# Kernel optimization log

Measured on AMD Instinct MI355X. Metric: run time of the kernel, lower is better.

Reference implementation:

```python
import jax, jax.numpy as jnp
import numpy as np

B, S, D = 8, 2048, 128
ALPHA = 1.0


def setup_inputs() -> dict:
    key = jax.random.key(0)
    kq, kk, kv, kl = jax.random.split(key, 4)
    q = jax.random.normal(kq, (B, S, D), dtype=jnp.float32)
    k = jax.random.normal(kk, (B, S, D), dtype=jnp.float32)
    v = jax.random.normal(kv, (B, S, D), dtype=jnp.float32)
    # ragged valid-length mask [B, S, 1] (1.0 for valid tokens) to exercise masked softmax
    lengths = jax.random.randint(kl, (B,), S // 2, S + 1)
    rep_mask = (jnp.arange(S)[None, :] < lengths[:, None]).astype(jnp.float32)[:, :, None]
    return {"q": q, "k": k, "v": v, "rep_mask": rep_mask}


def _masked_softmax(vec, mask):
    # faithful to torch masked_softmax with dim=2 (last axis)
    masked_vec = vec * mask
    max_vec = jnp.max(masked_vec, axis=2, keepdims=True)
    exps = jnp.exp(masked_vec - max_vec)
    masked_exps = exps * mask
    masked_sums = jnp.sum(masked_exps, axis=2, keepdims=True)
    masked_sums = masked_sums + (masked_sums == 0).astype(vec.dtype)
    return masked_exps / (masked_sums + 1e-20)


def reference(q, k, v, rep_mask):
    seq_len = q.shape[1]
    scale = jnp.sqrt(jnp.asarray(q.shape[2], dtype=q.dtype))
    attn = jnp.einsum('bsd,btd->bst', q, k) / scale  # [B,S,S]
    # rep mask tile: outer product of per-token validity
    mask = rep_mask * jnp.swapaxes(rep_mask, 1, 2)  # [B,S,S]
    # forward directional mask: strictly lower triangular (diagonal=-1)
    direct = jnp.tril(jnp.ones((seq_len, seq_len), dtype=q.dtype), k=-1)[None]
    mask = mask * direct
    # distance bias: -|i-j|
    idx = jnp.arange(seq_len)
    dist = -jnp.abs(idx[:, None] - idx[None, :]).astype(q.dtype)[None]
    attn = attn + ALPHA * dist
    attn = _masked_softmax(attn, mask)
    out = jnp.einsum('bst,btd->bsd', attn, v)  # [B,S,D]
    return (out, attn)
```

## Files before the change

### kernel.cpp

```cpp
#include <hip/hip_runtime.h>

#define NBATCH 8
#define S 2048
#define D 128
#define BQ 32
#define BK 64
#define NKT 32
#define NQT 64
#define INV_SQRT_D 0.08838834764831845f

typedef __bf16 bfv8 __attribute__((ext_vector_type(8)));
typedef float f32x4 __attribute__((ext_vector_type(4)));

__device__ __forceinline__ f32x4 mfma16(bfv8 a, bfv8 b, f32x4 c) {
    return __builtin_amdgcn_mfma_f32_16x16x32_bf16(a, b, c, 0, 0, 0);
}

__device__ __forceinline__ unsigned int pack2(float lo, float hi) {
    unsigned short a = __builtin_bit_cast(unsigned short, (__bf16)lo);
    unsigned short b = __builtin_bit_cast(unsigned short, (__bf16)hi);
    return (unsigned int)a | ((unsigned int)b << 16);
}

__device__ __forceinline__ void gload_lds16(const void* g, void* l) {
    __builtin_amdgcn_global_load_lds(
        (const __attribute__((address_space(1))) unsigned int*)g,
        (__attribute__((address_space(3))) unsigned int*)l, 16, 0, 0);
}

__global__ __launch_bounds__(256) void prep_kernel(
    const float* __restrict__ k, const float* __restrict__ v,
    __bf16* __restrict__ kb, __bf16* __restrict__ vtb)
{
    __shared__ __bf16 lds[64][132];
    const int bidx = blockIdx.x;
    const int tid  = threadIdx.x;

    if (bidx < 1024) {
        const int t   = bidx * 256 + tid;
        const int b   = t >> 15;
        const int kt  = (t >> 10) & 31;
        const int row = (t >> 4) & 63;
        const int u   = t & 15;
        const float4 f0 = *(const float4*)&k[((size_t)(b * S + kt * 64 + row)) * D + u * 8];
        const float4 f1 = *(const float4*)&k[((size_t)(b * S + kt * 64 + row)) * D + u * 8 + 4];
        bfv8 o;
        o[0] = (__bf16)f0.x; o[1] = (__bf16)f0.y; o[2] = (__bf16)f0.z; o[3] = (__bf16)f0.w;
        o[4] = (__bf16)f1.x; o[5] = (__bf16)f1.y; o[6] = (__bf16)f1.z; o[7] = (__bf16)f1.w;
        const size_t unit = ((size_t)((b * 32 + kt) * 64 + row)) * 16 + (u ^ (row & 7));
        *(bfv8*)&kb[unit * 8] = o;
    } else {
        const int vb = bidx - 1024;
        const int b  = vb >> 5;
        const int kt = vb & 31;
#pragma unroll
        for (int p = 0; p < 8; ++p) {
            const int idx = p * 256 + tid;
            const int kv  = idx >> 5;
            const int c4  = idx & 31;
            const float4 f = *(const float4*)&v[((size_t)(b * S + kt * 64 + kv)) * D + c4 * 4];
            __bf16* dst = &lds[kv][c4 * 4];
            dst[0] = (__bf16)f.x; dst[1] = (__bf16)f.y; dst[2] = (__bf16)f.z; dst[3] = (__bf16)f.w;
        }
        __syncthreads();
#pragma unroll
        for (int p = 0; p < 4; ++p) {
            const int idx = p * 256 + tid;
            const int d   = idx >> 3;
            const int u   = idx & 7;
            bfv8 o;
#pragma unroll
            for (int j = 0; j < 8; ++j) o[j] = lds[u * 8 + j][d];
            const size_t unit = ((size_t)((b * 32 + kt) * 128 + d)) * 8 + (u ^ (d & 7));
            *(bfv8*)&vtb[unit * 8] = o;
        }
    }
}

__global__ __launch_bounds__(256) void attn_main(
    const float* __restrict__ q, const float* __restrict__ rep,
    const __bf16* __restrict__ kb, const __bf16* __restrict__ vtb,
    float* __restrict__ out, float* __restrict__ attn)
{
    __shared__ __attribute__((aligned(16))) __bf16 slots[4][8192];
    __shared__ __attribute__((aligned(16))) __bf16 qs[BQ][136];
    __shared__ __attribute__((aligned(16))) __bf16 ps[BQ][72];
    __shared__ float redsum[2][2][16];
    __shared__ float dinv_lds[BQ];

    const int tid  = threadIdx.x;
    const int bid  = blockIdx.x;
    const int b    = bid & 7;
    const int g    = bid >> 3;
    const int qt   = (g < 32) ? (63 - g) : (g - 32);
    const int i0   = qt * BQ;
    const int NT   = ((qt * BQ + (BQ - 2)) >> 6) + 1;

    const int lane = tid & 63;
    const int w    = tid >> 6;
    const int rg   = w >> 1;
    const int ch   = w & 1;
    const int lr   = lane & 15;
    const int lg   = lane >> 4;

    auto stageK = [&](int kt, int slot) {
        const char* src = (const char*)kb + (((size_t)(b * 32 + kt)) << 14);
        char* dst = (char*)&slots[slot][0];
#pragma unroll
        for (int i2 = 0; i2 < 4; ++i2) {
            const int n0 = (w * 4 + i2) * 64;
            gload_lds16(src + (size_t)(n0 + lane) * 16, dst + (size_t)n0 * 16);
        }
    };
    auto stageV = [&](int kt, int slot) {
        const char* src = (const char*)vtb + (((size_t)(b * 32 + kt)) << 14);
        char* dst = (char*)&slots[slot][0];
#pragma unroll
        for (int i2 = 0; i2 < 4; ++i2) {
            const int n0 = (w * 4 + i2) * 64;
            gload_lds16(src + (size_t)(n0 + lane) * 16, dst + (size_t)n0 * 16);
        }
    };
    auto kfrag = [&](int slot, int row, int u) -> bfv8 {
        return *(const bfv8*)&slots[slot][(row * 16 + (u ^ (row & 7))) * 8];
    };
    auto vfrag = [&](int slot, int drow, int u) -> bfv8 {
        return *(const bfv8*)&slots[slot][(drow * 8 + (u ^ (drow & 7))) * 8];
    };

    stageK(0, 0);
    stageV(0, 2);

    for (int c = tid; c < BQ * 16; c += 256) {
        const int row = c >> 4, c8 = c & 15;
        const float4 f0 = *(const float4*)&q[((size_t)(b * S + i0 + row)) * D + c8 * 8];
        const float4 f1 = *(const float4*)&q[((size_t)(b * S + i0 + row)) * D + c8 * 8 + 4];
        bfv8 t;
        t[0] = (__bf16)f0.x; t[1] = (__bf16)f0.y; t[2] = (__bf16)f0.z; t[3] = (__bf16)f0.w;
        t[4] = (__bf16)f1.x; t[5] = (__bf16)f1.y; t[6] = (__bf16)f1.z; t[7] = (__bf16)f1.w;
        *(bfv8*)&qs[row][c8 * 8] = t;
    }

    unsigned int vm0 = 0, vm1 = 0;
    for (int kt = 0; kt < NT; ++kt) {
        const unsigned int t0 = (rep[(size_t)b * S + kt * BK + ch * 32 + lr]      > 0.5f) ? 1u : 0u;
        const unsigned int t1 = (rep[(size_t)b * S + kt * BK + ch * 32 + 16 + lr] > 0.5f) ? 1u : 0u;
        vm0 |= t0 << kt;
        vm1 |= t1 << kt;
    }

    int  i_r[4];
    bool bi[4];
#pragma unroll
    for (int r = 0; r < 4; ++r) {
        i_r[r] = i0 + rg * 16 + lg * 4 + r;
        bi[r]  = rep[(size_t)b * S + i_r[r]] > 0.5f;
    }
    __syncthreads();

    bfv8 qa[4];
#pragma unroll
    for (int ks = 0; ks < 4; ++ks)
        qa[ks] = *(const bfv8*)&qs[rg * 16 + lr][ks * 32 + lg * 8];

    const int krow = ch * 32 + lr;
    const int csw  = krow & 7;
    int koff[4];
#pragma unroll
    for (int ks = 0; ks < 4; ++ks)
        koff[ks] = krow * 256 + (((ks * 4 + lg) ^ csw) << 4);
    const char* kbb = (const char*)kb + (((size_t)(b * 32)) << 14);

    float lsum[4] = {0.f, 0.f, 0.f, 0.f};
#pragma unroll 2
    for (int kt = 0; kt < NT; ++kt) {
        const char* tp = kbb + ((size_t)kt << 14);
        bfv8 kf0[4], kf1[4];
#pragma unroll
        for (int ks = 0; ks < 4; ++ks) {
            kf0[ks] = *(const bfv8*)(tp + koff[ks]);
            kf1[ks] = *(const bfv8*)(tp + koff[ks] + 4096);
        }
        f32x4 acc0 = {0.f, 0.f, 0.f, 0.f}, acc1 = {0.f, 0.f, 0.f, 0.f};
#pragma unroll
        for (int ks = 0; ks < 4; ++ks) {
            acc0 = mfma16(qa[ks], kf0[ks], acc0);
            acc1 = mfma16(qa[ks], kf1[ks], acc1);
        }

        const int j0 = kt * BK + ch * 32 + lr;
        const int j1 = j0 + 16;
        const bool vj0 = (vm0 >> kt) & 1;
        const bool vj1 = (vm1 >> kt) & 1;
#pragma unroll
        for (int r = 0; r < 4; ++r) {
            const int i = i_r[r];
            const float p0 = (bi[r] && vj0 && (j0 < i))
                ? __expf(acc0[r] * INV_SQRT_D - (float)(i - j0)) : 0.f;
            const float p1 = (bi[r] && vj1 && (j1 < i))
                ? __expf(acc1[r] * INV_SQRT_D - (float)(i - j1)) : 0.f;
            lsum[r] += p0 + p1;
        }
    }

#pragma unroll
    for (int r = 0; r < 4; ++r) {
        lsum[r] += __shfl_xor(lsum[r], 1);
        lsum[r] += __shfl_xor(lsum[r], 2);
        lsum[r] += __shfl_xor(lsum[r], 4);
        lsum[r] += __shfl_xor(lsum[r], 8);
    }
    if (lr == 0) {
#pragma unroll
        for (int r = 0; r < 4; ++r) redsum[rg][ch][lg * 4 + r] = lsum[r];
    }
    __syncthreads();
    if (tid < BQ) {
        const float s = redsum[tid >> 4][0][tid & 15] + redsum[tid >> 4][1][tid & 15];
        dinv_lds[tid] = 1.f / (s + ((s == 0.f) ? 1.f : 0.f) + 1e-20f);
    }
    __syncthreads();

    float dinv[4];
#pragma unroll
    for (int r = 0; r < 4; ++r) dinv[r] = dinv_lds[rg * 16 + lg * 4 + r];

    f32x4 oacc[4];
#pragma unroll
    for (int nf = 0; nf < 4; ++nf) oacc[nf] = (f32x4){0.f, 0.f, 0.f, 0.f};

    for (int kt = 0; kt < NT; ++kt) {
        const int kslot = kt & 1;
        const int vslot = 2 + (kt & 1);

        if (kt + 1 < NT) { stageK(kt + 1, (kt + 1) & 1); stageV(kt + 1, 2 + ((kt + 1) & 1)); }

        f32x4 acc0 = {0.f, 0.f, 0.f, 0.f}, acc1 = {0.f, 0.f, 0.f, 0.f};
#pragma unroll
        for (int ks = 0; ks < 4; ++ks) {
            const bfv8 b0 = kfrag(kslot, ch * 32 + lr, ks * 4 + lg);
            const bfv8 b1 = kfrag(kslot, ch * 32 + 16 + lr, ks * 4 + lg);
            acc0 = mfma16(qa[ks], b0, acc0);
            acc1 = mfma16(qa[ks], b1, acc1);
        }

        const int j0 = kt * BK + ch * 32 + lr;
        const int j1 = j0 + 16;
        const bool vj0 = (vm0 >> kt) & 1;
        const bool vj1 = (vm1 >> kt) & 1;
#pragma unroll
        for (int r = 0; r < 4; ++r) {
            const int i = i_r[r];
            const float p0 = (bi[r] && vj0 && (j0 < i))
                ? __expf(acc0[r] * INV_SQRT_D - (float)(i - j0)) * dinv[r] : 0.f;
            const float p1 = (bi[r] && vj1 && (j1 < i))
                ? __expf(acc1[r] * INV_SQRT_D - (float)(i - j1)) * dinv[r] : 0.f;
            ps[rg * 16 + lg * 4 + r][ch * 32 + lr]      = (__bf16)p0;
            ps[rg * 16 + lg * 4 + r][ch * 32 + 16 + lr] = (__bf16)p1;
        }

        asm volatile("s_waitcnt lgkmcnt(0)" ::: "memory");
        __builtin_amdgcn_s_barrier();
        asm volatile("" ::: "memory");

        {
            const int arow = tid >> 3, ac = (tid & 7) * 8;
            const bfv8 t = *(const bfv8*)&ps[arow][ac];
            float4 f0, f1;
            f0.x = (float)t[0]; f0.y = (float)t[1]; f0.z = (float)t[2]; f0.w = (float)t[3];
            f1.x = (float)t[4]; f1.y = (float)t[5]; f1.z = (float)t[6]; f1.w = (float)t[7];
            float* ap = &attn[((size_t)(b * S + i0 + arow)) * S + kt * BK + ac];
            *(float4*)ap = f0;
            *(float4*)(ap + 4) = f1;
        }

#pragma unroll
        for (int ks = 0; ks < 2; ++ks) {
            const bfv8 pa = *(const bfv8*)&ps[rg * 16 + lr][ks * 32 + lg * 8];
#pragma unroll
            for (int nf = 0; nf < 4; ++nf) {
                const bfv8 vf = vfrag(vslot, ch * 64 + nf * 16 + lr, ks * 4 + lg);
                oacc[nf] = mfma16(pa, vf, oacc[nf]);
            }
        }

        asm volatile("s_waitcnt vmcnt(2)" ::: "memory");
        __builtin_amdgcn_s_barrier();
        asm volatile("" ::: "memory");
    }

#pragma unroll
    for (int nf = 0; nf < 4; ++nf)
#pragma unroll
        for (int r = 0; r < 4; ++r)
            out[((size_t)(b * S + i_r[r])) * D + ch * 64 + nf * 16 + lr] = oacc[nf][r];

    const int zt = NKT - NT;
    const float4 z4 = make_float4(0.f, 0.f, 0.f, 0.f);
    for (int u = tid; u < zt * 512; u += 256) {
        const int t   = u >> 9;
        const int rem = u & 511;
        const int row = rem >> 4;
        const int c4  = rem & 15;
        *(float4*)&attn[((size_t)(b * S + i0 + row)) * S + (NT + t) * BK + c4 * 4] = z4;
    }
}

__global__ __launch_bounds__(256) void attn_kernel_fb(
    const float* __restrict__ q, const float* __restrict__ k,
    const float* __restrict__ v, const float* __restrict__ rep,
    float* __restrict__ out, float* __restrict__ attn)
{
    __shared__ __attribute__((aligned(16))) __bf16 qs [BQ][136];
    __shared__ __attribute__((aligned(16))) __bf16 ksm[BK][136];
    __shared__ __attribute__((aligned(16))) __bf16 vsT[D][72];
    __shared__ __attribute__((aligned(16))) __bf16 psl[BQ][72];
    __shared__ float redsum[2][2][16];
    __shared__ float dinv_lds[BQ];

    const int tid  = threadIdx.x;
    const int bid  = blockIdx.x;
    const int b    = bid & 7;
    const int qt   = (NQT - 1) - (bid >> 3);
    const int i0   = qt * BQ;
    const int NT   = ((qt * BQ + (BQ - 2)) >> 6) + 1;

    const int lane = tid & 63;
    const int w    = tid >> 6;
    const int rg   = w >> 1;
    const int ch   = w & 1;
    const int lr   = lane & 15;
    const int lg   = lane >> 4;

    for (int c = tid; c < BQ * 16; c += 256) {
        const int row = c >> 4, c8 = c & 15;
        const float4 f0 = *(const float4*)&q[((size_t)(b * S + i0 + row)) * D + c8 * 8];
        const float4 f1 = *(const float4*)&q[((size_t)(b * S + i0 + row)) * D + c8 * 8 + 4];
        bfv8 t;
        t[0] = (__bf16)f0.x; t[1] = (__bf16)f0.y; t[2] = (__bf16)f0.z; t[3] = (__bf16)f0.w;
        t[4] = (__bf16)f1.x; t[5] = (__bf16)f1.y; t[6] = (__bf16)f1.z; t[7] = (__bf16)f1.w;
        *(bfv8*)&qs[row][c8 * 8] = t;
    }
    __syncthreads();

    bfv8 qa[4];
#pragma unroll
    for (int ks = 0; ks < 4; ++ks)
        qa[ks] = *(const bfv8*)&qs[rg * 16 + lr][ks * 32 + lg * 8];

    int  i_r[4];
    bool bi[4];
#pragma unroll
    for (int r = 0; r < 4; ++r) {
        i_r[r] = i0 + rg * 16 + lg * 4 + r;
        bi[r]  = rep[(size_t)b * S + i_r[r]] > 0.5f;
    }

    float lsum[4] = {0.f, 0.f, 0.f, 0.f};
    for (int kt = 0; kt < NT; ++kt) {
        __syncthreads();
        for (int c = tid; c < BK * 16; c += 256) {
            const int row = c >> 4, c8 = c & 15;
            const float4 f0 = *(const float4*)&k[((size_t)(b * S + kt * BK + row)) * D + c8 * 8];
            const float4 f1 = *(const float4*)&k[((size_t)(b * S + kt * BK + row)) * D + c8 * 8 + 4];
            bfv8 t;
            t[0] = (__bf16)f0.x; t[1] = (__bf16)f0.y; t[2] = (__bf16)f0.z; t[3] = (__bf16)f0.w;
            t[4] = (__bf16)f1.x; t[5] = (__bf16)f1.y; t[6] = (__bf16)f1.z; t[7] = (__bf16)f1.w;
            *(bfv8*)&ksm[row][c8 * 8] = t;
        }
        __syncthreads();

        f32x4 acc0 = {0.f, 0.f, 0.f, 0.f}, acc1 = {0.f, 0.f, 0.f, 0.f};
#pragma unroll
        for (int ks = 0; ks < 4; ++ks) {
            const bfv8 b0 = *(const bfv8*)&ksm[ch * 32 + lr][ks * 32 + lg * 8];
            const bfv8 b1 = *(const bfv8*)&ksm[ch * 32 + 16 + lr][ks * 32 + lg * 8];
            acc0 = mfma16(qa[ks], b0, acc0);
            acc1 = mfma16(qa[ks], b1, acc1);
        }
        const int j0 = kt * BK + ch * 32 + lr;
        const int j1 = j0 + 16;
        const bool vj0 = rep[(size_t)b * S + j0] > 0.5f;
        const bool vj1 = rep[(size_t)b * S + j1] > 0.5f;
#pragma unroll
        for (int r = 0; r < 4; ++r) {
            const int i = i_r[r];
            const float p0 = (bi[r] && vj0 && (j0 < i))
                ? __expf(acc0[r] * INV_SQRT_D - (float)(i - j0)) : 0.f;
            const float p1 = (bi[r] && vj1 && (j1 < i))
                ? __expf(acc1[r] * INV_SQRT_D - (float)(i - j1)) : 0.f;
            lsum[r] += p0 + p1;
        }
    }

#pragma unroll
    for (int r = 0; r < 4; ++r) {
        lsum[r] += __shfl_xor(lsum[r], 1);
        lsum[r] += __shfl_xor(lsum[r], 2);
        lsum[r] += __shfl_xor(lsum[r], 4);
        lsum[r] += __shfl_xor(lsum[r], 8);
    }
    if (lr == 0) {
#pragma unroll
        for (int r = 0; r < 4; ++r) redsum[rg][ch][lg * 4 + r] = lsum[r];
    }
    __syncthreads();
    if (tid < BQ) {
        const float s = redsum[tid >> 4][0][tid & 15] + redsum[tid >> 4][1][tid & 15];
        dinv_lds[tid] = 1.f / (s + ((s == 0.f) ? 1.f : 0.f) + 1e-20f);
    }
    __syncthreads();

    float dinv[4];
#pragma unroll
    for (int r = 0; r < 4; ++r) dinv[r] = dinv_lds[rg * 16 + lg * 4 + r];

    f32x4 oacc[4];
#pragma unroll
    for (int nf = 0; nf < 4; ++nf) oacc[nf] = (f32x4){0.f, 0.f, 0.f, 0.f};

    for (int kt = 0; kt < NT; ++kt) {
        __syncthreads();
        for (int c = tid; c < BK * 16; c += 256) {
            const int row = c >> 4, c8 = c & 15;
            const float4 f0 = *(const float4*)&k[((size_t)(b * S + kt * BK + row)) * D + c8 * 8];
            const float4 f1 = *(const float4*)&k[((size_t)(b * S + kt * BK + row)) * D + c8 * 8 + 4];
            bfv8 t;
            t[0] = (__bf16)f0.x; t[1] = (__bf16)f0.y; t[2] = (__bf16)f0.z; t[3] = (__bf16)f0.w;
            t[4] = (__bf16)f1.x; t[5] = (__bf16)f1.y; t[6] = (__bf16)f1.z; t[7] = (__bf16)f1.w;
            *(bfv8*)&ksm[row][c8 * 8] = t;
        }
        for (int u = tid; u < 1024; u += 256) {
            const int p  = u & 31;
            const int dq = u >> 5;
            const float4 va = *(const float4*)&v[((size_t)(b * S + kt * BK + 2 * p)) * D + dq * 4];
            const float4 vb = *(const float4*)&v[((size_t)(b * S + kt * BK + 2 * p + 1)) * D + dq * 4];
            *(unsigned int*)&vsT[dq * 4 + 0][2 * p] = pack2(va.x, vb.x);
            *(unsigned int*)&vsT[dq * 4 + 1][2 * p] = pack2(va.y, vb.y);
            *(unsigned int*)&vsT[dq * 4 + 2][2 * p] = pack2(va.z, vb.z);
            *(unsigned int*)&vsT[dq * 4 + 3][2 * p] = pack2(va.w, vb.w);
        }
        __syncthreads();

        f32x4 acc0 = {0.f, 0.f, 0.f, 0.f}, acc1 = {0.f, 0.f, 0.f, 0.f};
#pragma unroll
        for (int ks = 0; ks < 4; ++ks) {
            const bfv8 b0 = *(const bfv8*)&ksm[ch * 32 + lr][ks * 32 + lg * 8];
            const bfv8 b1 = *(const bfv8*)&ksm[ch * 32 + 16 + lr][ks * 32 + lg * 8];
            acc0 = mfma16(qa[ks], b0, acc0);
            acc1 = mfma16(qa[ks], b1, acc1);
        }
        const int j0 = kt * BK + ch * 32 + lr;
        const int j1 = j0 + 16;
        const bool vj0 = rep[(size_t)b * S + j0] > 0.5f;
        const bool vj1 = rep[(size_t)b * S + j1] > 0.5f;
#pragma unroll
        for (int r = 0; r < 4; ++r) {
            const int i = i_r[r];
            const float p0 = (bi[r] && vj0 && (j0 < i))
                ? __expf(acc0[r] * INV_SQRT_D - (float)(i - j0)) * dinv[r] : 0.f;
            const float p1 = (bi[r] && vj1 && (j1 < i))
                ? __expf(acc1[r] * INV_SQRT_D - (float)(i - j1)) * dinv[r] : 0.f;
            attn[((size_t)(b * S + i)) * S + j0] = p0;
            attn[((size_t)(b * S + i)) * S + j1] = p1;
            psl[rg * 16 + lg * 4 + r][ch * 32 + lr]      = (__bf16)p0;
            psl[rg * 16 + lg * 4 + r][ch * 32 + 16 + lr] = (__bf16)p1;
        }
        __syncthreads();

#pragma unroll
        for (int ks = 0; ks < 2; ++ks) {
            const bfv8 pa = *(const bfv8*)&psl[rg * 16 + lr][ks * 32 + lg * 8];
#pragma unroll
            for (int nf = 0; nf < 4; ++nf) {
                const bfv8 vf = *(const bfv8*)&vsT[ch * 64 + nf * 16 + lr][ks * 32 + lg * 8];
                oacc[nf] = mfma16(pa, vf, oacc[nf]);
            }
        }
    }

#pragma unroll
    for (int nf = 0; nf < 4; ++nf)
#pragma unroll
        for (int r = 0; r < 4; ++r)
            out[((size_t)(b * S + i_r[r])) * D + ch * 64 + nf * 16 + lr] = oacc[nf][r];

    const int zt = NKT - NT;
    const float4 z4 = make_float4(0.f, 0.f, 0.f, 0.f);
    for (int u = tid; u < zt * 512; u += 256) {
        const int t   = u >> 9;
        const int rem = u & 511;
        const int row = rem >> 4;
        const int c4  = rem & 15;
        *(float4*)&attn[((size_t)(b * S + i0 + row)) * S + (NT + t) * BK + c4 * 4] = z4;
    }
}

extern "C" void kernel_launch(void* const* d_in, const int* in_sizes, int n_in,
                              void* d_out, int out_size, void* d_ws, size_t ws_size,
                              hipStream_t stream)
{
    const float* q   = (const float*)d_in[0];
    const float* k   = (const float*)d_in[1];
    const float* v   = (const float*)d_in[2];
    const float* rep = (const float*)d_in[3];
    float* out  = (float*)d_out;
    float* attn = out + (size_t)NBATCH * S * D;

    const size_t kb_elems = (size_t)NBATCH * S * D;
    const size_t need = kb_elems * 2 * 2;

    if (ws_size < need) {
        hipLaunchKernelGGL(attn_kernel_fb, dim3(NBATCH * NQT), dim3(256), 0, stream,
                           q, k, v, rep, out, attn);
        return;
    }

    __bf16* kb  = (__bf16*)d_ws;
    __bf16* vtb = kb + kb_elems;

    hipLaunchKernelGGL(prep_kernel, dim3(1280), dim3(256), 0, stream, k, v, kb, vtb);
    hipLaunchKernelGGL(attn_main, dim3(NBATCH * NQT), dim3(256), 0, stream,
                       q, rep, kb, vtb, out, attn);
}
```

Before: 67.28 us.

## Fuse QK, exp and PV into a single pass with bf16 P scratch buffer

Adds a fused kernel that computes the unnormalized probabilities, accumulates P·V in the same key-tile loop, and stores bf16 P tiles to a workspace scratch buffer. After the row sums are known, it normalizes the output and rewrites attn from the scratch using nontemporal stores. This removes the separate second pass that recomputes QK^T and exp. In exchange it adds extra workspace traffic and needs a larger workspace. Without that workspace it falls back to the old path.

```diff
diff --git a/kernel.cpp b/kernel.cpp
--- a/kernel.cpp
+++ b/kernel.cpp
@@ -77,7 +77,194 @@
     }
 }
 
-__global__ __launch_bounds__(256) void attn_main(
+__global__ __launch_bounds__(256) void attn_fused(
+    const float* __restrict__ q, const float* __restrict__ rep,
+    const __bf16* __restrict__ kb, const __bf16* __restrict__ vtb,
+    __bf16* __restrict__ pws,
+    float* __restrict__ out, float* __restrict__ attn)
+{
+    __shared__ __attribute__((aligned(16))) __bf16 qs[BQ][136];
+    __shared__ __attribute__((aligned(16))) __bf16 ps[2][BQ][72];
+    __shared__ float redsum[2][2][16];
+    __shared__ float dinv_lds[BQ];
+
+    const int tid = threadIdx.x;
+    const int bid = blockIdx.x;
+    const int b   = bid & 7;
+    const int g   = bid >> 3;
+    const int qt  = (g < 32) ? (63 - g) : (g - 32);
+    const int i0  = qt * BQ;
+    const int NT  = ((qt * BQ + (BQ - 2)) >> 6) + 1;
+
+    const int lane = tid & 63;
+    const int w  = tid >> 6;
+    const int rg = w >> 1;
+    const int ch = w & 1;
+    const int lr = lane & 15;
+    const int lg = lane >> 4;
+
+    for (int c = tid; c < BQ * 16; c += 256) {
+        const int row = c >> 4, c8 = c & 15;
+        const float4 f0 = *(const float4*)&q[((size_t)(b * S + i0 + row)) * D + c8 * 8];
+        const float4 f1 = *(const float4*)&q[((size_t)(b * S + i0 + row)) * D + c8 * 8 + 4];
+        bfv8 t;
+        t[0] = (__bf16)f0.x; t[1] = (__bf16)f0.y; t[2] = (__bf16)f0.z; t[3] = (__bf16)f0.w;
+        t[4] = (__bf16)f1.x; t[5] = (__bf16)f1.y; t[6] = (__bf16)f1.z; t[7] = (__bf16)f1.w;
+        *(bfv8*)&qs[row][c8 * 8] = t;
+    }
+
+    unsigned int vm0 = 0, vm1 = 0;
+    for (int kt = 0; kt < NT; ++kt) {
+        const unsigned int t0 = (rep[(size_t)b * S + kt * BK + ch * 32 + lr]      > 0.5f) ? 1u : 0u;
+        const unsigned int t1 = (rep[(size_t)b * S + kt * BK + ch * 32 + 16 + lr] > 0.5f) ? 1u : 0u;
+        vm0 |= t0 << kt;
+        vm1 |= t1 << kt;
+    }
+
+    int  i_r[4];
+    bool bi[4];
+#pragma unroll
+    for (int r = 0; r < 4; ++r) {
+        i_r[r] = i0 + rg * 16 + lg * 4 + r;
+        bi[r]  = rep[(size_t)b * S + i_r[r]] > 0.5f;
+    }
+    __syncthreads();
+
+    bfv8 qa[4];
+#pragma unroll
+    for (int ks = 0; ks < 4; ++ks)
+        qa[ks] = *(const bfv8*)&qs[rg * 16 + lr][ks * 32 + lg * 8];
+
+    const int krow = ch * 32 + lr;
+    const int csw  = krow & 7;
+    int koff[4];
+#pragma unroll
+    for (int ks = 0; ks < 4; ++ks)
+        koff[ks] = krow * 256 + (((ks * 4 + lg) ^ csw) << 4);
+    const char* kbb = (const char*)kb + (((size_t)(b * 32)) << 14);
+
+    const int csv = lr & 7;
+    int voff[2][4];
+#pragma unroll
+    for (int ks = 0; ks < 2; ++ks)
+#pragma unroll
+        for (int nf = 0; nf < 4; ++nf)
+            voff[ks][nf] = (ch * 64 + nf * 16 + lr) * 128 + (((ks * 4 + lg) ^ csv) << 4);
+    const char* vbb = (const char*)vtb + (((size_t)(b * 32)) << 14);
+
+    const int h = qt >> 1;
+    const size_t ptile = (size_t)b * 1056 + (size_t)(qt + h * (h - 1 + (qt & 1)));
+    __bf16* pt = pws + ptile * 2048;
+
+    const int arow = tid >> 3;
+    const int ac   = (tid & 7) * 8;
+
+    float lsum[4] = {0.f, 0.f, 0.f, 0.f};
+    f32x4 oacc[4];
+#pragma unroll
+    for (int nf = 0; nf < 4; ++nf) oacc[nf] = (f32x4){0.f, 0.f, 0.f, 0.f};
+
+    for (int kt = 0; kt < NT; ++kt) {
+        const int pp = kt & 1;
+        const char* ktp = kbb + ((size_t)kt << 14);
+        const char* vtp = vbb + ((size_t)kt << 14);
+
+        bfv8 kf0[4], kf1[4];
+#pragma unroll
+        for (int ks = 0; ks < 4; ++ks) {
+            kf0[ks] = *(const bfv8*)(ktp + koff[ks]);
+            kf1[ks] = *(const bfv8*)(ktp + koff[ks] + 4096);
+        }
+        f32x4 acc0 = {0.f, 0.f, 0.f, 0.f}, acc1 = {0.f, 0.f, 0.f, 0.f};
+#pragma unroll
+        for (int ks = 0; ks < 4; ++ks) {
+            acc0 = mfma16(qa[ks], kf0[ks], acc0);
+            acc1 = mfma16(qa[ks], kf1[ks], acc1);
+        }
+
+        const int j0 = kt * BK + ch * 32 + lr;
+        const int j1 = j0 + 16;
+        const bool vj0 = (vm0 >> kt) & 1;
+        const bool vj1 = (vm1 >> kt) & 1;
+#pragma unroll
+        for (int r = 0; r < 4; ++r) {
+            const int i = i_r[r];
+            const float p0 = (bi[r] && vj0 && (j0 < i))
+                ? __expf(acc0[r] * INV_SQRT_D - (float)(i - j0)) : 0.f;
+            const float p1 = (bi[r] && vj1 && (j1 < i))
+                ? __expf(acc1[r] * INV_SQRT_D - (float)(i - j1)) : 0.f;
+            lsum[r] += p0 + p1;
+            ps[pp][rg * 16 + lg * 4 + r][ch * 32 + lr]      = (__bf16)p0;
+            ps[pp][rg * 16 + lg * 4 + r][ch * 32 + 16 + lr] = (__bf16)p1;
+        }
+
+        asm volatile("s_waitcnt lgkmcnt(0)" ::: "memory");
+        __builtin_amdgcn_s_barrier();
+        asm volatile("" ::: "memory");
+
+        *(bfv8*)(pt + (size_t)kt * 2048 + tid * 8) = *(const bfv8*)&ps[pp][arow][ac];
+
+#pragma unroll
+        for (int ks = 0; ks < 2; ++ks) {
+            const bfv8 pa = *(const bfv8*)&ps[pp][rg * 16 + lr][ks * 32 + lg * 8];
+#pragma unroll
+            for (int nf = 0; nf < 4; ++nf) {
+                const bfv8 vf = *(const bfv8*)(vtp + voff[ks][nf]);
+                oacc[nf] = mfma16(pa, vf, oacc[nf]);
+            }
+        }
+    }
+
+#pragma unroll
+    for (int r = 0; r < 4; ++r) {
+        lsum[r] += __shfl_xor(lsum[r], 1);
+        lsum[r] += __shfl_xor(lsum[r], 2);
+        lsum[r] += __shfl_xor(lsum[r], 4);
+        lsum[r] += __shfl_xor(lsum[r], 8);
+    }
+    if (lr == 0) {
+#pragma unroll
+        for (int r = 0; r < 4; ++r) redsum[rg][ch][lg * 4 + r] = lsum[r];
+    }
+    __syncthreads();
+    if (tid < BQ) {
+        const float s = redsum[tid >> 4][0][tid & 15] + redsum[tid >> 4][1][tid & 15];
+        dinv_lds[tid] = 1.f / (s + ((s == 0.f) ? 1.f : 0.f) + 1e-20f);
+    }
+    __syncthreads();
+
+    float dinv[4];
+#pragma unroll
+    for (int r = 0; r < 4; ++r) dinv[r] = dinv_lds[rg * 16 + lg * 4 + r];
+#pragma unroll
+    for (int nf = 0; nf < 4; ++nf)
+#pragma unroll
+        for (int r = 0; r < 4; ++r)
+            out[((size_t)(b * S + i_r[r])) * D + ch * 64 + nf * 16 + lr] = oacc[nf][r] * dinv[r];
+
+    const float rd = dinv_lds[arow];
+    float* aprow = &attn[((size_t)(b * S + i0 + arow)) * S + ac];
+#pragma unroll 4
+    for (int kt = 0; kt < NKT; ++kt) {
+        float* ap = aprow + kt * BK;
+        if (kt < NT) {
+            const bfv8 t = *(const bfv8*)(pt + (size_t)kt * 2048 + tid * 8);
+            f32x4 f0, f1;
+            f0[0] = (float)t[0] * rd; f0[1] = (float)t[1] * rd;
+            f0[2] = (float)t[2] * rd; f0[3] = (float)t[3] * rd;
+            f1[0] = (float)t[4] * rd; f1[1] = (float)t[5] * rd;
+            f1[2] = (float)t[6] * rd; f1[3] = (float)t[7] * rd;
+            __builtin_nontemporal_store(f0, (f32x4*)ap);
+            __builtin_nontemporal_store(f1, (f32x4*)(ap + 4));
+        } else {
+            const f32x4 z4 = {0.f, 0.f, 0.f, 0.f};
+            __builtin_nontemporal_store(z4, (f32x4*)ap);
+            __builtin_nontemporal_store(z4, (f32x4*)(ap + 4));
+        }
+    }
+}
+
+__global__ __launch_bounds__(256) void attn_main_mid(
     const float* __restrict__ q, const float* __restrict__ rep,
     const __bf16* __restrict__ kb, const __bf16* __restrict__ vtb,
     float* __restrict__ out, float* __restrict__ attn)
@@ -187,7 +374,6 @@
             acc0 = mfma16(qa[ks], kf0[ks], acc0);
             acc1 = mfma16(qa[ks], kf1[ks], acc1);
         }
-
         const int j0 = kt * BK + ch * 32 + lr;
         const int j1 = j0 + 16;
         const bool vj0 = (vm0 >> kt) & 1;
@@ -507,10 +693,12 @@
     float* out  = (float*)d_out;
     float* attn = out + (size_t)NBATCH * S * D;
 
-    const size_t kb_elems = (size_t)NBATCH * S * D;
-    const size_t need = kb_elems * 2 * 2;
-
-    if (ws_size < need) {
+    const size_t kb_elems  = (size_t)NBATCH * S * D;
+    const size_t need_mid  = kb_elems * 2 * 2;
+    const size_t p_bytes   = (size_t)NBATCH * 1056 * 4096;
+    const size_t need_full = need_mid + p_bytes;
+
+    if (ws_size < need_mid) {
         hipLaunchKernelGGL(attn_kernel_fb, dim3(NBATCH * NQT), dim3(256), 0, stream,
                            q, k, v, rep, out, attn);
         return;
@@ -520,6 +708,13 @@
     __bf16* vtb = kb + kb_elems;
 
     hipLaunchKernelGGL(prep_kernel, dim3(1280), dim3(256), 0, stream, k, v, kb, vtb);
-    hipLaunchKernelGGL(attn_main, dim3(NBATCH * NQT), dim3(256), 0, stream,
-                       q, rep, kb, vtb, out, attn);
+
+    if (ws_size >= need_full) {
+        __bf16* pws = vtb + kb_elems;
+        hipLaunchKernelGGL(attn_fused, dim3(NBATCH * NQT), dim3(256), 0, stream,
+                           q, rep, kb, vtb, pws, out, attn);
+    } else {
+        hipLaunchKernelGGL(attn_main_mid, dim3(NBATCH * NQT), dim3(256), 0, stream,
+                           q, rep, kb, vtb, out, attn);
+    }
 }
```

Measured after the change: 76.28 us. 1.13x slower.
